# Kernel optimization log

Measured on AMD Instinct MI355X. Metric: run time of the kernel, lower is better.

Reference implementation:

```python
import jax, jax.numpy as jnp
import numpy as np

B, N, CIN, K = 4, 4096, 64, 16
MLP = [64, 64, 128]
EPS = 1e-5


def setup_inputs() -> dict:
    key = jax.random.key(0)
    ks = jax.random.split(key, 8)
    inp = {
        "xyz": jax.random.normal(ks[0], (B, N, 3), dtype=jnp.float32),
        "points": jax.random.normal(ks[1], (B, N, CIN), dtype=jnp.float32),
    }
    last = 3 + CIN
    for i, oc in enumerate(MLP):
        inp[f"w{i}"] = jax.random.normal(ks[2 + i], (oc, last), dtype=jnp.float32) * 0.05
        inp[f"b{i}"] = jnp.zeros((oc,), dtype=jnp.float32)
        inp[f"g{i}"] = jnp.ones((oc,), dtype=jnp.float32)
        inp[f"be{i}"] = jnp.zeros((oc,), dtype=jnp.float32)
        inp[f"rm{i}"] = jnp.zeros((oc,), dtype=jnp.float32)
        inp[f"rv{i}"] = jnp.ones((oc,), dtype=jnp.float32)
        last = oc
    return inp


def reference(xyz, points, w0, b0, g0, be0, rm0, rv0,
              w1, b1, g1, be1, rm1, rv1,
              w2, b2, g2, be2, rm2, rv2):
    # knn via squared pairwise distance (same argsort order as cdist)
    sq = jnp.sum(xyz * xyz, axis=-1)  # (B,N)
    d2 = sq[:, :, None] + sq[:, None, :] - 2.0 * jnp.einsum('bnc,bmc->bnm', xyz, xyz)
    _, idx = jax.lax.top_k(-d2, K)  # (B,N,K), smallest-distance neighbors

    bidx = jnp.arange(xyz.shape[0])[:, None, None]  # (B,1,1)
    grouped_xyz = xyz[bidx, idx] - xyz[:, :, None, :]     # (B,N,K,3) relative coords
    grouped_pts = points[bidx, idx]                        # (B,N,K,CIN)
    h = jnp.concatenate([grouped_xyz, grouped_pts], axis=-1)  # (B,N,K,3+CIN)

    layers = [(w0, b0, g0, be0, rm0, rv0),
              (w1, b1, g1, be1, rm1, rv1),
              (w2, b2, g2, be2, rm2, rv2)]
    for (w, b, g, be, rm, rv) in layers:
        # 1x1 conv == per-point linear; BN in eval mode (running stats)
        h = jnp.einsum('bnkc,oc->bnko', h, w) + b
        h = (h - rm) * jax.lax.rsqrt(rv + EPS) * g + be
        h = jax.nn.relu(h)
    new_points = jnp.max(h, axis=2)  # max over K neighbors -> (B,N,C_out)
    return new_points
```

## Files before the change

### kernel.cpp

```cpp
#include <hip/hip_runtime.h>

#define NPT   4096
#define KNN_K 16
#define EPSV  1e-5f

#define W1T_OFF 4352
#define B1_OFF  8448
#define W2T_OFF 8512
#define B2_OFF  16704
#define IDX_OFF 16832
#define P_OFF   344512
#define Q_OFF   1393088

typedef unsigned long long ull;

__device__ __forceinline__ ull minu64(ull a, ull b) { return a < b ? a : b; }
__device__ __forceinline__ ull maxu64(ull a, ull b) { return a > b ? a : b; }

__device__ __forceinline__ ull bitonic_sort64(ull v, int lane) {
#pragma unroll
  for (int k = 2; k <= 64; k <<= 1) {
#pragma unroll
    for (int j = k >> 1; j > 0; j >>= 1) {
      ull o = __shfl_xor(v, j);
      bool lower = (lane & j) == 0;
      bool up = (lane & k) == 0;
      v = (lower == up) ? minu64(v, o) : maxu64(v, o);
    }
  }
  return v;
}

__device__ __forceinline__ ull bitonic_merge64(ull v, int lane) {
#pragma unroll
  for (int j = 32; j > 0; j >>= 1) {
    ull o = __shfl_xor(v, j);
    v = ((lane & j) == 0) ? minu64(v, o) : maxu64(v, o);
  }
  return v;
}

__global__ __launch_bounds__(256) void mega_kernel(
    const float* __restrict__ xyz, const float* __restrict__ points,
    const float* __restrict__ w0, const float* __restrict__ b0, const float* __restrict__ g0,
    const float* __restrict__ be0, const float* __restrict__ rm0, const float* __restrict__ rv0,
    const float* __restrict__ w1, const float* __restrict__ b1, const float* __restrict__ g1,
    const float* __restrict__ be1, const float* __restrict__ rm1, const float* __restrict__ rv1,
    const float* __restrict__ w2, const float* __restrict__ b2, const float* __restrict__ g2,
    const float* __restrict__ be2, const float* __restrict__ rm2, const float* __restrict__ rv2,
    float* __restrict__ ws, int* __restrict__ knnOut) {
  __shared__ __align__(16) unsigned char smem[20480];
  int blk = blockIdx.x;
  int tid = threadIdx.x;

  if (blk < 4096) {
    float4* tile = (float4*)smem;
    ull* buf = (ull*)(smem + 16384);
    int lane = tid & 63, w = tid >> 6;
    int b = blk >> 10;
    int n = ((blk & 1023) << 2) + w;
    const float* xb = xyz + (size_t)b * NPT * 3;

    float4 q;
    {
      const float* qp = xb + n * 3;
      float qx = qp[0], qy = qp[1], qz = qp[2];
      float qsq = __fadd_rn(__fadd_rn(__fmul_rn(qx, qx), __fmul_rn(qy, qy)),
                            __fmul_rn(qz, qz));
      q = make_float4(qx, qy, qz, qsq);
    }
    ull R = ~0ull;
    ull thresh = ~0ull;
    int cnt = 0;
    ull ltmask = (lane == 0) ? 0ull : (~0ull >> (64 - lane));
    const float4* r4 = (const float4*)xb;

#pragma unroll 1
    for (int t = 0; t < 4; ++t) {
      __syncthreads();
      {
        int fo = 768 * t + 3 * tid;
        float4 A = r4[fo], B = r4[fo + 1], C = r4[fo + 2];
        float xs[4] = {A.x, A.w, B.z, C.y};
        float ys[4] = {A.y, B.x, B.w, C.z};
        float zs[4] = {A.z, B.y, C.x, C.w};
#pragma unroll
        for (int j = 0; j < 4; ++j) {
          float sq = __fadd_rn(__fadd_rn(__fmul_rn(xs[j], xs[j]), __fmul_rn(ys[j], ys[j])),
                               __fmul_rn(zs[j], zs[j]));
          tile[4 * tid + j] = make_float4(xs[j], ys[j], zs[j], sq);
        }
      }
      __syncthreads();
#pragma unroll 1
      for (int i = 0; i < 16; ++i) {
        int ml = (i << 6) + lane;
        float4 c = tile[ml];
        float dot = __fadd_rn(__fadd_rn(__fmul_rn(q.x, c.x), __fmul_rn(q.y, c.y)),
                              __fmul_rn(q.z, c.z));
        float d2 = __fsub_rn(__fadd_rn(q.w, c.w), __fmul_rn(2.0f, dot));
        unsigned bits = __float_as_uint(d2);
        unsigned fk = bits ^ (0x80000000u | (unsigned)((int)bits >> 31));
        ull key = ((ull)fk << 32) | (unsigned)((t << 10) + ml);
        bool pred = key < thresh;
        ull mask = __ballot(pred);
        if (mask) {
          int pos = cnt + __popcll(mask & ltmask);
          if (pred) buf[w * 128 + pos] = key;
          cnt += __popcll(mask);
          if (cnt >= 64) {
            ull v = buf[w * 128 + lane];
            v = bitonic_sort64(v, lane);
            ull vr = __shfl(v, 63 - lane);
            R = minu64(R, vr);
            R = bitonic_merge64(R, lane);
            thresh = __shfl(R, 15);
            cnt -= 64;
            if (lane < cnt) {
              ull tmp = buf[w * 128 + 64 + lane];
              buf[w * 128 + lane] = tmp;
            }
          }
        }
      }
    }
    {
      ull v = (lane < cnt) ? buf[w * 128 + lane] : ~0ull;
      v = bitonic_sort64(v, lane);
      ull vr = __shfl(v, 63 - lane);
      R = minu64(R, vr);
      R = bitonic_merge64(R, lane);
    }
    if (lane < KNN_K)
      knnOut[(b * NPT + n) * KNN_K + lane] = (int)(unsigned)(R & 0xFFFFFFFFull);
    return;
  }

  if (blk < 8192) {
    float* wlds = (float*)smem;
    for (int j = tid; j < 4288; j += 256) wlds[j] = w0[j];
    __syncthreads();
    int oc = tid & 63;
    int i = (blk - 4096) * 4 + (tid >> 6);
    float s = g0[oc] * rsqrtf(rv0[oc] + EPSV);
    float b0f = (b0[oc] - rm0[oc]) * s + be0[oc];
    const float* wrow = wlds + oc * 67;
    float x = xyz[i * 3], y = xyz[i * 3 + 1], z = xyz[i * 3 + 2];
    float qacc = __fmul_rn(wrow[0], s) * x;
    qacc = fmaf(__fmul_rn(wrow[1], s), y, qacc);
    qacc = fmaf(__fmul_rn(wrow[2], s), z, qacc);
    float acc = b0f + qacc;
    const float* prow = points + (size_t)i * 64;
#pragma unroll 4
    for (int c = 0; c < 64; ++c)
      acc = fmaf(__fmul_rn(wrow[3 + c], s), prow[c], acc);
    ws[P_OFF + (size_t)i * 64 + oc] = acc;
    ws[Q_OFF + (size_t)i * 64 + oc] = qacc;
    return;
  }

  {
    int i = (blk - 8192) * 256 + tid + 4352;
    if (i < 8448) {
      int j = i - 4352; int oc = j & 63, ic = j >> 6;
      float s = g1[oc] * rsqrtf(rv1[oc] + EPSV);
      ws[i] = w1[oc * 64 + ic] * s;
    } else if (i < 8512) {
      int oc = i - 8448;
      float s = g1[oc] * rsqrtf(rv1[oc] + EPSV);
      ws[i] = (b1[oc] - rm1[oc]) * s + be1[oc];
    } else if (i < 16704) {
      int j = i - 8512; int ic = j >> 7, oc = j & 127;
      float s = g2[oc] * rsqrtf(rv2[oc] + EPSV);
      ws[i] = w2[oc * 64 + ic] * s;
    } else if (i < 16832) {
      int oc = i - 16704;
      float s = g2[oc] * rsqrtf(rv2[oc] + EPSV);
      ws[i] = (b2[oc] - rm2[oc]) * s + be2[oc];
    }
  }
}

__global__ __launch_bounds__(256) void mlp_kernel(
    const float* __restrict__ wbuf, const int* __restrict__ knn,
    float* __restrict__ out) {
  __shared__ __align__(16) float Ash[64 * 128];
  __shared__ __align__(16) float Wsh[64 * 64];
  int tid = threadIdx.x;
  int qblk = blockIdx.x << 3;

  const float4* w1g = (const float4*)(wbuf + W1T_OFF);
  float4 st0 = w1g[tid];
  float4 st1 = w1g[256 + tid];
  float4 st2 = w1g[512 + tid];
  float4 st3 = w1g[768 + tid];

  {
    int p = tid & 127, half = tid >> 7;
    int q = qblk + (p >> 4);
    int k = p & 15;
    int src = knn[q * KNN_K + k];
    int srow = (q & ~(NPT - 1)) + src;
    const float4* Pp = (const float4*)(wbuf + P_OFF + (size_t)srow * 64 + half * 32);
    const float4* Qp = (const float4*)(wbuf + Q_OFF + (size_t)q * 64 + half * 32);
#pragma unroll
    for (int j = 0; j < 8; ++j) {
      float4 pv = Pp[j];
      float4 qv = Qp[j];
      int ic = half * 32 + j * 4;
      Ash[(ic + 0) * 128 + p] = fmaxf(pv.x - qv.x, 0.0f);
      Ash[(ic + 1) * 128 + p] = fmaxf(pv.y - qv.y, 0.0f);
      Ash[(ic + 2) * 128 + p] = fmaxf(pv.z - qv.z, 0.0f);
      Ash[(ic + 3) * 128 + p] = fmaxf(pv.w - qv.w, 0.0f);
    }
  }
  {
    float4* wl = (float4*)Wsh;
    wl[tid] = st0; wl[256 + tid] = st1; wl[512 + tid] = st2; wl[768 + tid] = st3;
  }
  const float4* w2g = (const float4*)(wbuf + W2T_OFF);
  {
    int r0 = tid, r1 = 256 + tid, r2 = 512 + tid, r3 = 768 + tid;
    st0 = w2g[(r0 >> 4) * 32 + (r0 & 15)];
    st1 = w2g[(r1 >> 4) * 32 + (r1 & 15)];
    st2 = w2g[(r2 >> 4) * 32 + (r2 & 15)];
    st3 = w2g[(r3 >> 4) * 32 + (r3 & 15)];
  }
  __syncthreads();

  int og = tid & 7, pg = tid >> 3;
  const float* Arow = Ash + 4 * pg;
  const float* Wrow = Wsh + 8 * og;
  float acc[4][8];

  {
    float4 b0v = *(const float4*)(wbuf + B1_OFF + 8 * og);
    float4 b1v = *(const float4*)(wbuf + B1_OFF + 8 * og + 4);
    float bj[8] = {b0v.x, b0v.y, b0v.z, b0v.w, b1v.x, b1v.y, b1v.z, b1v.w};
#pragma unroll
    for (int i = 0; i < 4; ++i)
#pragma unroll
      for (int j = 0; j < 8; ++j) acc[i][j] = bj[j];
#pragma unroll 8
    for (int ic = 0; ic < 64; ++ic) {
      float4 a0 = *(const float4*)(Arow + ic * 128);
      float4 w0v = *(const float4*)(Wrow + ic * 64);
      float4 w1v = *(const float4*)(Wrow + ic * 64 + 4);
      float av[4] = {a0.x, a0.y, a0.z, a0.w};
      float wv[8] = {w0v.x, w0v.y, w0v.z, w0v.w, w1v.x, w1v.y, w1v.z, w1v.w};
#pragma unroll
      for (int i = 0; i < 4; ++i)
#pragma unroll
        for (int j = 0; j < 8; ++j) acc[i][j] = fmaf(av[i], wv[j], acc[i][j]);
    }
  }
  __syncthreads();
#pragma unroll
  for (int j = 0; j < 8; ++j) {
    int oc = 8 * og + j;
    *(float4*)(Ash + oc * 128 + 4 * pg) =
        make_float4(fmaxf(acc[0][j], 0.0f), fmaxf(acc[1][j], 0.0f),
                    fmaxf(acc[2][j], 0.0f), fmaxf(acc[3][j], 0.0f));
  }
  {
    float4* wl = (float4*)Wsh;
    wl[tid] = st0; wl[256 + tid] = st1; wl[512 + tid] = st2; wl[768 + tid] = st3;
    int r0 = tid, r1 = 256 + tid, r2 = 512 + tid, r3 = 768 + tid;
    st0 = w2g[(r0 >> 4) * 32 + 16 + (r0 & 15)];
    st1 = w2g[(r1 >> 4) * 32 + 16 + (r1 & 15)];
    st2 = w2g[(r2 >> 4) * 32 + 16 + (r2 & 15)];
    st3 = w2g[(r3 >> 4) * 32 + 16 + (r3 & 15)];
  }
  __syncthreads();

  int qout = qblk + (pg >> 2);
  float* obase = out + (size_t)qout * 128 + 8 * og;
#pragma unroll 1
  for (int pass = 0; pass < 2; ++pass) {
    {
      float4 b0v = *(const float4*)(wbuf + B2_OFF + pass * 64 + 8 * og);
      float4 b1v = *(const float4*)(wbuf + B2_OFF + pass * 64 + 8 * og + 4);
      float bj[8] = {b0v.x, b0v.y, b0v.z, b0v.w, b1v.x, b1v.y, b1v.z, b1v.w};
#pragma unroll
      for (int i = 0; i < 4; ++i)
#pragma unroll
        for (int j = 0; j < 8; ++j) acc[i][j] = bj[j];
    }
#pragma unroll 8
    for (int ic = 0; ic < 64; ++ic) {
      float4 a0 = *(const float4*)(Arow + ic * 128);
      float4 w0v = *(const float4*)(Wrow + ic * 64);
      float4 w1v = *(const float4*)(Wrow + ic * 64 + 4);
      float av[4] = {a0.x, a0.y, a0.z, a0.w};
      float wv[8] = {w0v.x, w0v.y, w0v.z, w0v.w, w1v.x, w1v.y, w1v.z, w1v.w};
#pragma unroll
      for (int i = 0; i < 4; ++i)
#pragma unroll
        for (int j = 0; j < 8; ++j) acc[i][j] = fmaf(av[i], wv[j], acc[i][j]);
    }
    float m[8];
#pragma unroll
    for (int j = 0; j < 8; ++j) {
      float v = fmaxf(fmaxf(acc[0][j], acc[1][j]), fmaxf(acc[2][j], acc[3][j]));
      v = fmaxf(v, 0.0f);
      v = fmaxf(v, __shfl_xor(v, 8));
      m[j] = fmaxf(v, __shfl_xor(v, 16));
    }
    if ((pg & 3) == 0) {
      *(float4*)(obase + pass * 64)     = make_float4(m[0], m[1], m[2], m[3]);
      *(float4*)(obase + pass * 64 + 4) = make_float4(m[4], m[5], m[6], m[7]);
    }
    if (pass == 0) {
      __syncthreads();
      float4* wl = (float4*)Wsh;
      wl[tid] = st0; wl[256 + tid] = st1; wl[512 + tid] = st2; wl[768 + tid] = st3;
      __syncthreads();
    }
  }
}

extern "C" void kernel_launch(void* const* d_in, const int* in_sizes, int n_in,
                              void* d_out, int out_size, void* d_ws, size_t ws_size,
                              hipStream_t stream) {
  const float* xyz    = (const float*)d_in[0];
  const float* points = (const float*)d_in[1];
  float* wsF = (float*)d_ws;
  int* idxBuf = (int*)(wsF + IDX_OFF);

  mega_kernel<<<8241, 256, 0, stream>>>(
      xyz, points,
      (const float*)d_in[2],  (const float*)d_in[3],  (const float*)d_in[4],
      (const float*)d_in[5],  (const float*)d_in[6],  (const float*)d_in[7],
      (const float*)d_in[8],  (const float*)d_in[9],  (const float*)d_in[10],
      (const float*)d_in[11], (const float*)d_in[12], (const float*)d_in[13],
      (const float*)d_in[14], (const float*)d_in[15], (const float*)d_in[16],
      (const float*)d_in[17], (const float*)d_in[18], (const float*)d_in[19],
      wsF, idxBuf);
  mlp_kernel<<<2048, 256, 0, stream>>>(wsF, idxBuf, (float*)d_out);
}
```

Measured before the change: 266.0 us.

## Interleave kNN and layer-0 blocks, simplify kNN key filter, halve MLP weight LDS

kNN blocks and layer-0 projection blocks now alternate by block parity, so the two workloads share CUs instead of running in separate phases. The kNN inner loop compares only the 32-bit distance key against the threshold, builds the full 64-bit key only for accepted candidates, and uses mbcnt to compute lane prefix counts. The MLP kernel stages weights in 32-row halves, which shrinks the weight LDS buffer, and sets launch bounds to 4 blocks per SM to raise occupancy. The cost is extra barriers per GEMM and more candidates passing when distances tie.

Result: slower. 321.2 us (+20.8%).

```diff
diff --git a/kernel.cpp b/kernel.cpp
--- a/kernel.cpp
+++ b/kernel.cpp
@@ -53,12 +53,13 @@
   int blk = blockIdx.x;
   int tid = threadIdx.x;
 
-  if (blk < 4096) {
+  if (blk < 8192 && (blk & 1) == 0) {
+    int kb = blk >> 1;
     float4* tile = (float4*)smem;
     ull* buf = (ull*)(smem + 16384);
     int lane = tid & 63, w = tid >> 6;
-    int b = blk >> 10;
-    int n = ((blk & 1023) << 2) + w;
+    int b = kb >> 10;
+    int n = ((kb & 1023) << 2) + w;
     const float* xb = xyz + (size_t)b * NPT * 3;
 
     float4 q;
@@ -70,9 +71,8 @@
       q = make_float4(qx, qy, qz, qsq);
     }
     ull R = ~0ull;
-    ull thresh = ~0ull;
+    unsigned thresh_hi = 0xFFFFFFFFu;
     int cnt = 0;
-    ull ltmask = (lane == 0) ? 0ull : (~0ull >> (64 - lane));
     const float4* r4 = (const float4*)xb;
 
 #pragma unroll 1
@@ -94,19 +94,21 @@
       __syncthreads();
 #pragma unroll 1
       for (int i = 0; i < 16; ++i) {
-        int ml = (i << 6) + lane;
-        float4 c = tile[ml];
+        float4 c = tile[(i << 6) + lane];
         float dot = __fadd_rn(__fadd_rn(__fmul_rn(q.x, c.x), __fmul_rn(q.y, c.y)),
                               __fmul_rn(q.z, c.z));
         float d2 = __fsub_rn(__fadd_rn(q.w, c.w), __fmul_rn(2.0f, dot));
         unsigned bits = __float_as_uint(d2);
         unsigned fk = bits ^ (0x80000000u | (unsigned)((int)bits >> 31));
-        ull key = ((ull)fk << 32) | (unsigned)((t << 10) + ml);
-        bool pred = key < thresh;
+        bool pred = fk <= thresh_hi;
         ull mask = __ballot(pred);
         if (mask) {
-          int pos = cnt + __popcll(mask & ltmask);
-          if (pred) buf[w * 128 + pos] = key;
+          int pos = cnt + (int)__builtin_amdgcn_mbcnt_hi(
+                              (unsigned)(mask >> 32),
+                              __builtin_amdgcn_mbcnt_lo((unsigned)mask, 0u));
+          if (pred)
+            buf[w * 128 + pos] =
+                ((ull)fk << 32) | (unsigned)((t << 10) + (i << 6) + lane);
           cnt += __popcll(mask);
           if (cnt >= 64) {
             ull v = buf[w * 128 + lane];
@@ -114,7 +116,7 @@
             ull vr = __shfl(v, 63 - lane);
             R = minu64(R, vr);
             R = bitonic_merge64(R, lane);
-            thresh = __shfl(R, 15);
+            thresh_hi = (unsigned)__shfl((int)(unsigned)(R >> 32), 15);
             cnt -= 64;
             if (lane < cnt) {
               ull tmp = buf[w * 128 + 64 + lane];
@@ -141,7 +143,7 @@
     for (int j = tid; j < 4288; j += 256) wlds[j] = w0[j];
     __syncthreads();
     int oc = tid & 63;
-    int i = (blk - 4096) * 4 + (tid >> 6);
+    int i = (blk >> 1) * 4 + (tid >> 6);
     float s = g0[oc] * rsqrtf(rv0[oc] + EPSV);
     float b0f = (b0[oc] - rm0[oc]) * s + be0[oc];
     const float* wrow = wlds + oc * 67;
@@ -181,19 +183,22 @@
   }
 }
 
-__global__ __launch_bounds__(256) void mlp_kernel(
+__global__ __launch_bounds__(256, 4) void mlp_kernel(
     const float* __restrict__ wbuf, const int* __restrict__ knn,
     float* __restrict__ out) {
   __shared__ __align__(16) float Ash[64 * 128];
-  __shared__ __align__(16) float Wsh[64 * 64];
+  __shared__ __align__(16) float Wsh[32 * 64];
   int tid = threadIdx.x;
   int qblk = blockIdx.x << 3;
 
   const float4* w1g = (const float4*)(wbuf + W1T_OFF);
-  float4 st0 = w1g[tid];
-  float4 st1 = w1g[256 + tid];
-  float4 st2 = w1g[512 + tid];
-  float4 st3 = w1g[768 + tid];
+  const float4* w2g = (const float4*)(wbuf + W2T_OFF);
+  float4* wl = (float4*)Wsh;
+
+#define W2IDX(e, p, h) ((((h) << 5) + ((e) >> 4)) * 32 + ((p) << 4) + ((e) & 15))
+
+  float4 s0 = w1g[tid];
+  float4 s1 = w1g[256 + tid];
 
   {
     int p = tid & 127, half = tid >> 7;
@@ -214,18 +219,8 @@
       Ash[(ic + 3) * 128 + p] = fmaxf(pv.w - qv.w, 0.0f);
     }
   }
-  {
-    float4* wl = (float4*)Wsh;
-    wl[tid] = st0; wl[256 + tid] = st1; wl[512 + tid] = st2; wl[768 + tid] = st3;
-  }
-  const float4* w2g = (const float4*)(wbuf + W2T_OFF);
-  {
-    int r0 = tid, r1 = 256 + tid, r2 = 512 + tid, r3 = 768 + tid;
-    st0 = w2g[(r0 >> 4) * 32 + (r0 & 15)];
-    st1 = w2g[(r1 >> 4) * 32 + (r1 & 15)];
-    st2 = w2g[(r2 >> 4) * 32 + (r2 & 15)];
-    st3 = w2g[(r3 >> 4) * 32 + (r3 & 15)];
-  }
+  wl[tid] = s0; wl[256 + tid] = s1;
+  s0 = w1g[512 + tid]; s1 = w1g[768 + tid];
   __syncthreads();
 
   int og = tid & 7, pg = tid >> 3;
@@ -233,6 +228,20 @@
   const float* Wrow = Wsh + 8 * og;
   float acc[4][8];
 
+#define GEMM32(R0)                                                        \
+  _Pragma("unroll 8")                                                     \
+  for (int ic = 0; ic < 32; ++ic) {                                       \
+    float4 a0 = *(const float4*)(Arow + ((R0) + ic) * 128);               \
+    float4 wv0 = *(const float4*)(Wrow + ic * 64);                        \
+    float4 wv1 = *(const float4*)(Wrow + ic * 64 + 4);                    \
+    float av[4] = {a0.x, a0.y, a0.z, a0.w};                               \
+    float wv[8] = {wv0.x, wv0.y, wv0.z, wv0.w, wv1.x, wv1.y, wv1.z, wv1.w};\
+    _Pragma("unroll")                                                     \
+    for (int ii = 0; ii < 4; ++ii)                                        \
+      _Pragma("unroll")                                                   \
+      for (int jj = 0; jj < 8; ++jj) acc[ii][jj] = fmaf(av[ii], wv[jj], acc[ii][jj]); \
+  }
+
   {
     float4 b0v = *(const float4*)(wbuf + B1_OFF + 8 * og);
     float4 b1v = *(const float4*)(wbuf + B1_OFF + 8 * og + 4);
@@ -241,20 +250,15 @@
     for (int i = 0; i < 4; ++i)
 #pragma unroll
       for (int j = 0; j < 8; ++j) acc[i][j] = bj[j];
-#pragma unroll 8
-    for (int ic = 0; ic < 64; ++ic) {
-      float4 a0 = *(const float4*)(Arow + ic * 128);
-      float4 w0v = *(const float4*)(Wrow + ic * 64);
-      float4 w1v = *(const float4*)(Wrow + ic * 64 + 4);
-      float av[4] = {a0.x, a0.y, a0.z, a0.w};
-      float wv[8] = {w0v.x, w0v.y, w0v.z, w0v.w, w1v.x, w1v.y, w1v.z, w1v.w};
-#pragma unroll
-      for (int i = 0; i < 4; ++i)
-#pragma unroll
-        for (int j = 0; j < 8; ++j) acc[i][j] = fmaf(av[i], wv[j], acc[i][j]);
-    }
-  }
-  __syncthreads();
+  }
+  GEMM32(0)
+  __syncthreads();
+  wl[tid] = s0; wl[256 + tid] = s1;
+  s0 = w2g[W2IDX(tid, 0, 0)]; s1 = w2g[W2IDX(tid + 256, 0, 0)];
+  __syncthreads();
+  GEMM32(32)
+  __syncthreads();
+
 #pragma unroll
   for (int j = 0; j < 8; ++j) {
     int oc = 8 * og + j;
@@ -262,42 +266,29 @@
         make_float4(fmaxf(acc[0][j], 0.0f), fmaxf(acc[1][j], 0.0f),
                     fmaxf(acc[2][j], 0.0f), fmaxf(acc[3][j], 0.0f));
   }
-  {
-    float4* wl = (float4*)Wsh;
-    wl[tid] = st0; wl[256 + tid] = st1; wl[512 + tid] = st2; wl[768 + tid] = st3;
-    int r0 = tid, r1 = 256 + tid, r2 = 512 + tid, r3 = 768 + tid;
-    st0 = w2g[(r0 >> 4) * 32 + 16 + (r0 & 15)];
-    st1 = w2g[(r1 >> 4) * 32 + 16 + (r1 & 15)];
-    st2 = w2g[(r2 >> 4) * 32 + 16 + (r2 & 15)];
-    st3 = w2g[(r3 >> 4) * 32 + 16 + (r3 & 15)];
-  }
+  wl[tid] = s0; wl[256 + tid] = s1;
+  s0 = w2g[W2IDX(tid, 0, 1)]; s1 = w2g[W2IDX(tid + 256, 0, 1)];
   __syncthreads();
 
   int qout = qblk + (pg >> 2);
   float* obase = out + (size_t)qout * 128 + 8 * og;
-#pragma unroll 1
-  for (int pass = 0; pass < 2; ++pass) {
-    {
-      float4 b0v = *(const float4*)(wbuf + B2_OFF + pass * 64 + 8 * og);
-      float4 b1v = *(const float4*)(wbuf + B2_OFF + pass * 64 + 8 * og + 4);
-      float bj[8] = {b0v.x, b0v.y, b0v.z, b0v.w, b1v.x, b1v.y, b1v.z, b1v.w};
-#pragma unroll
-      for (int i = 0; i < 4; ++i)
-#pragma unroll
-        for (int j = 0; j < 8; ++j) acc[i][j] = bj[j];
-    }
-#pragma unroll 8
-    for (int ic = 0; ic < 64; ++ic) {
-      float4 a0 = *(const float4*)(Arow + ic * 128);
-      float4 w0v = *(const float4*)(Wrow + ic * 64);
-      float4 w1v = *(const float4*)(Wrow + ic * 64 + 4);
-      float av[4] = {a0.x, a0.y, a0.z, a0.w};
-      float wv[8] = {w0v.x, w0v.y, w0v.z, w0v.w, w1v.x, w1v.y, w1v.z, w1v.w};
-#pragma unroll
-      for (int i = 0; i < 4; ++i)
-#pragma unroll
-        for (int j = 0; j < 8; ++j) acc[i][j] = fmaf(av[i], wv[j], acc[i][j]);
-    }
+
+  {
+    float4 b0v = *(const float4*)(wbuf + B2_OFF + 8 * og);
+    float4 b1v = *(const float4*)(wbuf + B2_OFF + 8 * og + 4);
+    float bj[8] = {b0v.x, b0v.y, b0v.z, b0v.w, b1v.x, b1v.y, b1v.z, b1v.w};
+#pragma unroll
+    for (int i = 0; i < 4; ++i)
+#pragma unroll
+      for (int j = 0; j < 8; ++j) acc[i][j] = bj[j];
+  }
+  GEMM32(0)
+  __syncthreads();
+  wl[tid] = s0; wl[256 + tid] = s1;
+  s0 = w2g[W2IDX(tid, 1, 0)]; s1 = w2g[W2IDX(tid + 256, 1, 0)];
+  __syncthreads();
+  GEMM32(32)
+  {
     float m[8];
 #pragma unroll
     for (int j = 0; j < 8; ++j) {
@@ -307,16 +298,45 @@
       m[j] = fmaxf(v, __shfl_xor(v, 16));
     }
     if ((pg & 3) == 0) {
-      *(float4*)(obase + pass * 64)     = make_float4(m[0], m[1], m[2], m[3]);
-      *(float4*)(obase + pass * 64 + 4) = make_float4(m[4], m[5], m[6], m[7]);
-    }
-    if (pass == 0) {
-      __syncthreads();
-      float4* wl = (float4*)Wsh;
-      wl[tid] = st0; wl[256 + tid] = st1; wl[512 + tid] = st2; wl[768 + tid] = st3;
-      __syncthreads();
-    }
-  }
+      *(float4*)(obase)     = make_float4(m[0], m[1], m[2], m[3]);
+      *(float4*)(obase + 4) = make_float4(m[4], m[5], m[6], m[7]);
+    }
+  }
+  __syncthreads();
+  wl[tid] = s0; wl[256 + tid] = s1;
+  s0 = w2g[W2IDX(tid, 1, 1)]; s1 = w2g[W2IDX(tid + 256, 1, 1)];
+  __syncthreads();
+
+  {
+    float4 b0v = *(const float4*)(wbuf + B2_OFF + 64 + 8 * og);
+    float4 b1v = *(const float4*)(wbuf + B2_OFF + 64 + 8 * og + 4);
+    float bj[8] = {b0v.x, b0v.y, b0v.z, b0v.w, b1v.x, b1v.y, b1v.z, b1v.w};
+#pragma unroll
+    for (int i = 0; i < 4; ++i)
+#pragma unroll
+      for (int j = 0; j < 8; ++j) acc[i][j] = bj[j];
+  }
+  GEMM32(0)
+  __syncthreads();
+  wl[tid] = s0; wl[256 + tid] = s1;
+  __syncthreads();
+  GEMM32(32)
+  {
+    float m[8];
+#pragma unroll
+    for (int j = 0; j < 8; ++j) {
+      float v = fmaxf(fmaxf(acc[0][j], acc[1][j]), fmaxf(acc[2][j], acc[3][j]));
+      v = fmaxf(v, 0.0f);
+      v = fmaxf(v, __shfl_xor(v, 8));
+      m[j] = fmaxf(v, __shfl_xor(v, 16));
+    }
+    if ((pg & 3) == 0) {
+      *(float4*)(obase + 64)     = make_float4(m[0], m[1], m[2], m[3]);
+      *(float4*)(obase + 64 + 4) = make_float4(m[4], m[5], m[6], m[7]);
+    }
+  }
+#undef GEMM32
+#undef W2IDX
 }
 
 extern "C" void kernel_launch(void* const* d_in, const int* in_sizes, int n_in,
```
